# Performance work log

Hardware: AMD Instinct MI355X
Metric: run time of the kernel (lower is better)

Reference implementation:

```python
import math
import jax, jax.numpy as jnp
import numpy as np

B, S, D, H = 2, 2048, 1024, 16
HD = D // H  # 64
EPS = 1e-5


def _layernorm(x, g, b):
    mu = jnp.mean(x, axis=-1, keepdims=True)
    var = jnp.mean(jnp.square(x - mu), axis=-1, keepdims=True)
    return (x - mu) * jax.lax.rsqrt(var + EPS) * g + b


def setup_inputs() -> dict:
    key = jax.random.key(0)
    ks = jax.random.split(key, 16)
    s_attn = 1.0 / math.sqrt(D)
    s_mlp = 1.0 / math.sqrt(4 * D)
    return {
        "hidden_states": jax.random.normal(ks[0], (B, S, D), jnp.float32),
        # MHA params (torch Linear convention: y = x @ W.T + b)
        "Wqkv": jax.random.normal(ks[1], (3 * D, D), jnp.float32) * s_attn,
        "bqkv": jax.random.normal(ks[2], (3 * D,), jnp.float32) * s_attn,
        "Wout": jax.random.normal(ks[3], (D, D), jnp.float32) * s_attn,
        "bout": jax.random.normal(ks[4], (D,), jnp.float32) * s_attn,
        # LayerNorms
        "g1": jnp.ones((D,), jnp.float32),
        "b1": jnp.zeros((D,), jnp.float32),
        "g2": jnp.ones((D,), jnp.float32),
        "b2": jnp.zeros((D,), jnp.float32),
        # MLP (hidden = 4*D, activation = tanh)
        "W1": jax.random.normal(ks[5], (4 * D, D), jnp.float32) * s_attn,
        "bfc1": jax.random.normal(ks[6], (4 * D,), jnp.float32) * s_attn,
        "W2": jax.random.normal(ks[7], (D, 4 * D), jnp.float32) * s_mlp,
        "bfc2": jax.random.normal(ks[8], (D,), jnp.float32) * s_mlp,
    }


def _mha(x, Wqkv, bqkv, Wout, bout):
    # qkv: (B,S,3,H,hd)
    qkv = (x @ Wqkv.T + bqkv).reshape(B, S, 3, H, HD)
    q, k, v = qkv[:, :, 0], qkv[:, :, 1], qkv[:, :, 2]
    # NOTE: source einsum 'bshd,btjd->bsht' contracts over k's head axis j,
    # so each query head attends against sum-over-heads of K (and of V).
    k_sum = k.sum(axis=2)  # (B,S,hd)
    v_sum = v.sum(axis=2)  # (B,S,hd)
    scale = 1.0 / math.sqrt(HD)
    scores = jnp.einsum('bshd,btd->bsht', q, k_sum) * scale  # (B,S,H,S)
    causal = jnp.triu(jnp.ones((S, S), bool), k=1)  # True above diagonal
    scores = jnp.where(causal[None, :, None, :], -jnp.inf, scores)
    attn = jax.nn.softmax(scores, axis=-1)
    out = jnp.einsum('bsht,btd->bshd', attn, v_sum).reshape(B, S, D)
    return out @ Wout.T + bout


def reference(hidden_states, Wqkv, bqkv, Wout, bout, g1, b1, g2, b2, W1, bfc1, W2, bfc2):
    # eval mode: dropouts and stochastic-depth are identity
    residual = hidden_states
    h = _layernorm(residual, g1, b1)
    h = _mha(h, Wqkv, bqkv, Wout, bout)
    residual = h + residual
    h = _layernorm(residual, g2, b2)
    h = jnp.tanh(h @ W1.T + bfc1) @ W2.T + bfc2
    return (h, residual)
```

## Files before the change

kernel.cpp:

```cpp
#include <hip/hip_runtime.h>
#include <hip/hip_bf16.h>

typedef __attribute__((ext_vector_type(8))) short s16x8;
typedef __attribute__((ext_vector_type(4))) float f32x4;
typedef __hip_bfloat16 bf16_t;

__device__ __forceinline__ void gload_lds16(const void* g, void* l) {
  __builtin_amdgcn_global_load_lds(
      (__attribute__((address_space(1))) void*)(g),
      (__attribute__((address_space(3))) void*)(l), 16, 0, 0);
}

__device__ __forceinline__ unsigned cvt_pk_bf16(float lo, float hi) {
  unsigned r;
  asm("v_cvt_pk_bf16_f32 %0, %1, %2" : "=v"(r) : "v"(lo), "v"(hi));
  return r;
}

__device__ __forceinline__ float fast_tanh(float x) {
  float t = exp2f(x * 2.885390082f);
  return 1.0f - 2.0f * __builtin_amdgcn_rcpf(t + 1.0f);
}

__global__ void cast_all_k(const float* __restrict__ Wqkv, const float* __restrict__ Wout,
                           const float* __restrict__ W1, const float* __restrict__ W2,
                           bf16_t* __restrict__ Wqkv_bf, bf16_t* __restrict__ Wout_bf,
                           bf16_t* __restrict__ W1_bf, bf16_t* __restrict__ W2_bf) {
  int c = blockIdx.x * 256 + threadIdx.x;
  const float* src; bf16_t* dst; int off;
  if (c < 131072)      { src = Wqkv; dst = Wqkv_bf; off = c; }
  else if (c < 262144) { src = Wout; dst = Wout_bf; off = c - 131072; }
  else if (c < 786432) { src = W1;   dst = W1_bf;   off = c - 262144; }
  else                 { src = W2;   dst = W2_bf;   off = c - 786432; }
  int i = off * 8;
  float4 a = *(const float4*)(src + i);
  float4 b = *(const float4*)(src + i + 4);
  union { bf16_t h[8]; s16x8 v; } u;
  u.h[0] = __float2bfloat16(a.x); u.h[1] = __float2bfloat16(a.y);
  u.h[2] = __float2bfloat16(a.z); u.h[3] = __float2bfloat16(a.w);
  u.h[4] = __float2bfloat16(b.x); u.h[5] = __float2bfloat16(b.y);
  u.h[6] = __float2bfloat16(b.z); u.h[7] = __float2bfloat16(b.w);
  *(s16x8*)(dst + i) = u.v;
}

__global__ void reduce_kv_k(const float* __restrict__ Wqkv, bf16_t* __restrict__ Wred) {
  int d   = blockIdx.x & 63;
  int isv = blockIdx.x >> 6;
  int col = threadIdx.x * 4;
  const float* base = Wqkv + (size_t)(1024 + isv * 1024 + d) * 1024 + col;
  float4 s = {0.f, 0.f, 0.f, 0.f};
#pragma unroll
  for (int h = 0; h < 16; ++h) {
    float4 t = *(const float4*)(base + (size_t)h * 64 * 1024);
    s.x += t.x; s.y += t.y; s.z += t.z; s.w += t.w;
  }
  union { bf16_t h[4]; uint2 u; } o;
  o.h[0] = __float2bfloat16(s.x); o.h[1] = __float2bfloat16(s.y);
  o.h[2] = __float2bfloat16(s.z); o.h[3] = __float2bfloat16(s.w);
  *(uint2*)(Wred + (size_t)(isv * 64 + d) * 1024 + col) = o.u;
}

__global__ void bias_prep_k(const float* __restrict__ bqkv, float* __restrict__ br) {
  int i = blockIdx.x * 256 + threadIdx.x;
  if (i >= 1152) return;
  if (i < 1024) { br[i] = bqkv[i]; return; }
  int d = i - 1024;
  int off = (d < 64) ? (1024 + d) : (2048 + (d - 64));
  float s = 0.f;
#pragma unroll
  for (int h = 0; h < 16; ++h) s += bqkv[off + h * 64];
  br[i] = s;
}

__global__ __launch_bounds__(256) void ln_cast_k(const float* __restrict__ x,
                                                 const float* __restrict__ g,
                                                 const float* __restrict__ bb,
                                                 bf16_t* __restrict__ y) {
  int row = blockIdx.x, tid = threadIdx.x;
  float4 v = *(const float4*)(x + (size_t)row * 1024 + tid * 4);
  float s = v.x + v.y + v.z + v.w;
  float q = v.x * v.x + v.y * v.y + v.z * v.z + v.w * v.w;
#pragma unroll
  for (int off = 1; off < 64; off <<= 1) {
    s += __shfl_xor(s, off, 64);
    q += __shfl_xor(q, off, 64);
  }
  __shared__ float ss[4], qq[4];
  int wave = tid >> 6, lane = tid & 63;
  if (lane == 0) { ss[wave] = s; qq[wave] = q; }
  __syncthreads();
  s = ss[0] + ss[1] + ss[2] + ss[3];
  q = qq[0] + qq[1] + qq[2] + qq[3];
  float mu  = s * (1.0f / 1024.0f);
  float var = q * (1.0f / 1024.0f) - mu * mu;
  float rstd = rsqrtf(var + 1e-5f);
  float4 gg = *(const float4*)(g + tid * 4);
  float4 bv = *(const float4*)(bb + tid * 4);
  union { bf16_t h[4]; uint2 u; } o;
  o.h[0] = __float2bfloat16((v.x - mu) * rstd * gg.x + bv.x);
  o.h[1] = __float2bfloat16((v.y - mu) * rstd * gg.y + bv.y);
  o.h[2] = __float2bfloat16((v.z - mu) * rstd * gg.z + bv.z);
  o.h[3] = __float2bfloat16((v.w - mu) * rstd * gg.w + bv.w);
  *(uint2*)(y + (size_t)row * 1024 + tid * 4) = o.u;
}

template <int EPI>
__global__ __launch_bounds__(512) void gemm256(
    const bf16_t* __restrict__ A, const bf16_t* __restrict__ Bw,
    const float* __restrict__ bias, void* __restrict__ out0,
    int M, int N, int K, int Kslice) {
  __shared__ __align__(16) bf16_t As[2 * 16384];
  __shared__ __align__(16) bf16_t Bs[2 * 16384];
  const int tid  = threadIdx.x;
  const int lane = tid & 63;
  const int wave = tid >> 6;
  const int l15 = lane & 15, lg = lane >> 4;
  const int wm = wave >> 2, wn = wave & 3;

  const unsigned nx = gridDim.x, ny = gridDim.y;
  unsigned fid = (blockIdx.z * ny + blockIdx.y) * nx + blockIdx.x;
  const unsigned nwg = nx * ny * gridDim.z;
  fid = (fid & 7) * (nwg >> 3) + (fid >> 3);
  const unsigned bxu = fid % nx;
  const unsigned rem = fid / nx;
  const unsigned byu = rem % ny;
  const unsigned bzu = rem / ny;
  const int bm = byu * 256, bn = bxu * 256;
  const size_t Kz = (size_t)K;
  const int kstart = bzu * Kslice;

  f32x4 acc[8][4];
#pragma unroll
  for (int f = 0; f < 8; ++f)
#pragma unroll
    for (int g = 0; g < 4; ++g) acc[f][g] = (f32x4){0.f, 0.f, 0.f, 0.f};

  const bf16_t* Ab = A + (size_t)bm * Kz + kstart;
  const bf16_t* Bb = Bw + (size_t)bn * Kz + kstart;

  const int srow = (tid & 7);
  auto stage = [&](int t, int buf) {
    const int k0 = t * 64;
#pragma unroll
    for (int j = 0; j < 4; ++j) {
      const int c   = j * 512 + tid;
      const int row = c >> 3;
      const int kc  = (c & 7) ^ (row & 7);
      gload_lds16(Ab + (size_t)row * Kz + k0 + kc * 8,
                  As + buf * 16384 + (j * 512 + wave * 64) * 8);
      gload_lds16(Bb + (size_t)row * Kz + k0 + kc * 8,
                  Bs + buf * 16384 + (j * 512 + wave * 64) * 8);
    }
  };
  (void)srow;

  const int NT = Kslice >> 6;
  stage(0, 0);
  int buf = 0;
  for (int t = 0; t < NT; ++t) {
    asm volatile("s_waitcnt vmcnt(0)" ::: "memory");
    __builtin_amdgcn_s_barrier();
    if (t + 1 < NT) stage(t + 1, buf ^ 1);
#pragma unroll
    for (int h = 0; h < 2; ++h) {
      s16x8 af[8], bfv[4];
#pragma unroll
      for (int f = 0; f < 8; ++f) {
        const int row = wm * 128 + f * 16 + l15;
        af[f] = *(const s16x8*)&As[buf * 16384 + (row * 8 + ((h * 4 + lg) ^ (l15 & 7))) * 8];
      }
#pragma unroll
      for (int g = 0; g < 4; ++g) {
        const int row = wn * 64 + g * 16 + l15;
        bfv[g] = *(const s16x8*)&Bs[buf * 16384 + (row * 8 + ((h * 4 + lg) ^ (l15 & 7))) * 8];
      }
      __builtin_amdgcn_s_setprio(1);
#pragma unroll
      for (int f = 0; f < 8; ++f)
#pragma unroll
        for (int g = 0; g < 4; ++g)
          acc[f][g] = __builtin_amdgcn_mfma_f32_16x16x32_bf16(af[f], bfv[g], acc[f][g], 0, 0, 0);
      __builtin_amdgcn_s_setprio(0);
    }
    buf ^= 1;
  }

#pragma unroll
  for (int f = 0; f < 8; ++f) {
    const int row0 = bm + wm * 128 + f * 16 + lg * 4;
#pragma unroll
    for (int g = 0; g < 4; ++g) {
      const int col = bn + wn * 64 + g * 16 + l15;
      const float bcol = (EPI == 4) ? 0.f : bias[col];
#pragma unroll
      for (int r = 0; r < 4; ++r) {
        const int rw = row0 + r;
        float c = acc[f][g][r] + bcol;
        if constexpr (EPI == 2) {
          ((bf16_t*)out0)[(size_t)rw * N + col] = __float2bfloat16(fast_tanh(c));
        } else {
          ((bf16_t*)out0)[((size_t)bzu * M + rw) * N + col] = __float2bfloat16(c);
        }
      }
    }
  }
}

template <int EPI>
__global__ __launch_bounds__(256) void gemm64(
    const bf16_t* __restrict__ A, const bf16_t* __restrict__ Bw,
    const float* __restrict__ bias, void* __restrict__ out0,
    const float* __restrict__ resid, bf16_t* __restrict__ oks,
    bf16_t* __restrict__ ovt, int M, int N, int K) {
  __shared__ __align__(16) bf16_t As[2 * 64 * 32];
  __shared__ __align__(16) bf16_t Bs[2 * 128 * 32];
  const int tid  = threadIdx.x;
  const int lane = tid & 63;
  const int wave = tid >> 6;
  const int l15 = lane & 15, lg = lane >> 4;
  const int wr = (wave >> 1) * 32, wc = (wave & 1) * 64;
  const int bm = blockIdx.y * 64, bn = blockIdx.x * 128;
  const size_t Kz = (size_t)K;
  const int srow = lane >> 2;
  const int scol = ((lane & 3) ^ ((lane >> 3) & 3)) * 8;

  f32x4 acc[2][4];
#pragma unroll
  for (int m = 0; m < 2; ++m)
#pragma unroll
    for (int n = 0; n < 4; ++n) acc[m][n] = (f32x4){0.f, 0.f, 0.f, 0.f};

  const bf16_t* Ab = A + (size_t)bm * Kz;
  const bf16_t* Bb = Bw + (size_t)bn * Kz;

  auto stage = [&](int t, int buf) {
    const int k0 = t * 32;
    gload_lds16(Ab + (size_t)(wave * 16 + srow) * Kz + k0 + scol, As + buf * 2048 + wave * 512);
#pragma unroll
    for (int j = 0; j < 2; ++j) {
      const int cw = wave * 2 + j;
      gload_lds16(Bb + (size_t)(cw * 16 + srow) * Kz + k0 + scol, Bs + buf * 4096 + cw * 512);
    }
  };

  const int NT = K >> 5;
  const int rdoff = (lg ^ ((l15 >> 1) & 3)) * 8;
  stage(0, 0);
  __syncthreads();
  int buf = 0;
  for (int t = 0; t < NT; ++t) {
    if (t + 1 < NT) stage(t + 1, buf ^ 1);
    s16x8 af[2], bfv[4];
#pragma unroll
    for (int m = 0; m < 2; ++m)
      af[m] = *(const s16x8*)&As[buf * 2048 + (wr + m * 16 + l15) * 32 + rdoff];
#pragma unroll
    for (int n = 0; n < 4; ++n)
      bfv[n] = *(const s16x8*)&Bs[buf * 4096 + (wc + n * 16 + l15) * 32 + rdoff];
#pragma unroll
    for (int m = 0; m < 2; ++m)
#pragma unroll
      for (int n = 0; n < 4; ++n)
        acc[m][n] = __builtin_amdgcn_mfma_f32_16x16x32_bf16(af[m], bfv[n], acc[m][n], 0, 0, 0);
    __syncthreads();
    buf ^= 1;
  }

#pragma unroll
  for (int m = 0; m < 2; ++m) {
    const int row0 = bm + wr + m * 16 + lg * 4;
#pragma unroll
    for (int n = 0; n < 4; ++n) {
      const int col = bn + wc + n * 16 + l15;
      const float bcol = bias[col];
#pragma unroll
      for (int r = 0; r < 4; ++r) {
        const int rw = row0 + r;
        float c = acc[m][n][r] + bcol;
        if constexpr (EPI == 0) {
          if (col < 1024) {
            ((bf16_t*)out0)[(size_t)rw * 1024 + col] =
                __float2bfloat16(c * 0.1803368801f);
          } else if (col < 1088) {
            int d = col - 1024, b = rw >> 11, t = rw & 2047;
            oks[((size_t)(b << 11) + t) * 64 + d] = __float2bfloat16(c);
          } else {
            int d = col - 1088, b = rw >> 11, t = rw & 2047;
            ovt[((size_t)b * 64 + d) * 2048 + t] = __float2bfloat16(c);
          }
        } else {
          ((float*)out0)[(size_t)rw * N + col] = c + resid[(size_t)rw * N + col];
        }
      }
    }
  }
}

__global__ __launch_bounds__(256) void fc2_reduce_k(const bf16_t* __restrict__ p,
                                                    const float* __restrict__ bias,
                                                    float* __restrict__ out) {
  const size_t PL = (size_t)4096 * 1024;
  size_t i = ((size_t)blockIdx.x * 256 + threadIdx.x) * 8;
  float acc[8];
  {
    union { s16x8 v; bf16_t h[8]; } u;
    u.v = *(const s16x8*)(p + i);
#pragma unroll
    for (int j = 0; j < 8; ++j) acc[j] = __bfloat162float(u.h[j]);
  }
#pragma unroll
  for (int z = 1; z < 4; ++z) {
    union { s16x8 v; bf16_t h[8]; } u;
    u.v = *(const s16x8*)(p + z * PL + i);
#pragma unroll
    for (int j = 0; j < 8; ++j) acc[j] += __bfloat162float(u.h[j]);
  }
  const int col = (int)(i & 1023);
#pragma unroll
  for (int j = 0; j < 8; ++j) acc[j] += bias[col + j];
  *(float4*)(out + i)     = (float4){acc[0], acc[1], acc[2], acc[3]};
  *(float4*)(out + i + 4) = (float4){acc[4], acc[5], acc[6], acc[7]};
}


template <bool MASK>
__device__ __forceinline__ void attn_tile(
    int t0, int p, const s16x8 (&qf)[2],
    const bf16_t* __restrict__ Ks, const bf16_t* __restrict__ Vs,
    bf16_t* __restrict__ Pl, int l15, int lg,
    float& m_run, float& l_part, f32x4 (&ao)[4]) {
  const int sw7 = l15 & 7;

  f32x4 sc[4];
#pragma unroll
  for (int n = 0; n < 4; ++n) sc[n] = (f32x4){0.f, 0.f, 0.f, 0.f};
#pragma unroll
  for (int ks2 = 0; ks2 < 2; ++ks2) {
#pragma unroll
    for (int n = 0; n < 4; ++n) {
      s16x8 kf = *(const s16x8*)&Ks[(n * 16 + l15) * 64 + (((ks2 << 2) | lg) ^ sw7) * 8];
      sc[n] = __builtin_amdgcn_mfma_f32_16x16x32_bf16(kf, qf[ks2], sc[n], 0, 0, 0);
    }
  }

  float mx = -1e30f;
#pragma unroll
  for (int n = 0; n < 4; ++n) {
#pragma unroll
    for (int r = 0; r < 4; ++r) {
      float v = sc[n][r];
      if (MASK && (t0 + n * 16 + lg * 4 + r > p)) v = -1e30f;
      sc[n][r] = v;
      mx = fmaxf(mx, v);
    }
  }
  if (__any(mx > m_run + 11.5f)) {
    float mxf = fmaxf(mx, __shfl_xor(mx, 16, 64));
    mxf = fmaxf(mxf, __shfl_xor(mxf, 32, 64));
    float mn = fmaxf(m_run, mxf);
    float alpha = exp2f(m_run - mn);
    m_run = mn;
    l_part *= alpha;
#pragma unroll
    for (int r = 0; r < 4; ++r) {
      float ar = __shfl(alpha, lg * 4 + r, 64);
#pragma unroll
      for (int n2 = 0; n2 < 4; ++n2) ao[n2][r] *= ar;
    }
  }
#pragma unroll
  for (int n = 0; n < 4; ++n) {
    float e0 = exp2f(sc[n][0] - m_run);
    float e1 = exp2f(sc[n][1] - m_run);
    float e2 = exp2f(sc[n][2] - m_run);
    float e3 = exp2f(sc[n][3] - m_run);
    l_part += (e0 + e1) + (e2 + e3);
    uint2 d;
    d.x = cvt_pk_bf16(e0, e1);
    d.y = cvt_pk_bf16(e2, e3);
    *(uint2*)&Pl[l15 * 72 + n * 16 + lg * 4] = d;
  }
#pragma unroll
  for (int ks2 = 0; ks2 < 2; ++ks2) {
    s16x8 pa = *(const s16x8*)&Pl[l15 * 72 + ks2 * 32 + lg * 8];
#pragma unroll
    for (int n2 = 0; n2 < 4; ++n2) {
      s16x8 vf = *(const s16x8*)&Vs[(n2 * 16 + l15) * 64 + (((ks2 << 2) | lg) ^ sw7) * 8];
      ao[n2] = __builtin_amdgcn_mfma_f32_16x16x32_bf16(pa, vf, ao[n2], 0, 0, 0);
    }
  }
}

__global__ __launch_bounds__(512) void attn_k(const bf16_t* __restrict__ q,
                                              const bf16_t* __restrict__ ksp,
                                              const bf16_t* __restrict__ vtp,
                                              bf16_t* __restrict__ o) {
  __shared__ __align__(16) bf16_t Ks[3 * 4096];
  __shared__ __align__(16) bf16_t Vs[3 * 4096];
  __shared__ __align__(16) bf16_t Plds[8][16 * 72];
  const int tid = threadIdx.x, lane = tid & 63, wave = tid >> 6;
  const int l15 = lane & 15, lg = lane >> 4;
  const int grp = blockIdx.x >> 1;
  const int b   = blockIdx.x & 1;
  const int pbase = 2040 - 8 * grp;
  const int p = pbase + wave;

  const bf16_t* qb_b = q   + (size_t)b * 32768 * 64;
  const bf16_t* ksb  = ksp + (size_t)b * 2048 * 64;
  const bf16_t* vtb  = vtp + (size_t)b * 64 * 2048;
  bf16_t*       ob   = o   + (size_t)b * 32768 * 64;
  bf16_t* Pl = &Plds[wave][0];

  const int srow = lane >> 3;
  const int scol = lane & 7;
  const int grow = wave * 8 + srow;
  const int gcol = scol ^ (grow & 7);
  const bf16_t* ksrc0 = ksb + (size_t)grow * 64 + gcol * 8;
  const bf16_t* vsrc0 = vtb + (size_t)grow * 2048 + gcol * 8;

  auto stageKV = [&](int t, int buf) {
    const int t0 = t * 64;
    gload_lds16(ksrc0 + (size_t)t0 * 64, Ks + buf * 4096 + wave * 512);
    gload_lds16(vsrc0 + t0, Vs + buf * 4096 + wave * 512);
  };

  s16x8 qf[2];
  {
    const bf16_t* qptr = qb_b + (size_t)(16 * p + l15) * 64;
    qf[0] = *(const s16x8*)(qptr + lg * 8);
    qf[1] = *(const s16x8*)(qptr + 32 + lg * 8);
  }

  float m_run = -1e30f, l_part = 0.f;
  f32x4 ao[4];
#pragma unroll
  for (int n = 0; n < 4; ++n) ao[n] = (f32x4){0.f, 0.f, 0.f, 0.f};

  const int nst = (pbase + 71) >> 6;
  stageKV(0, 0);
  if (nst > 1) stageKV(1, 1);
  int b0 = 0, b1 = 1, b2 = 2;
  for (int tt = 0; tt < nst; ++tt) {
    if (tt + 1 < nst) asm volatile("s_waitcnt vmcnt(2)" ::: "memory");
    else              asm volatile("s_waitcnt vmcnt(0)" ::: "memory");
    __builtin_amdgcn_s_barrier();
    if (tt + 2 < nst) stageKV(tt + 2, b2);
    const int t0 = tt * 64;
    if (t0 <= p) {
      const bf16_t* Kc = Ks + b0 * 4096;
      const bf16_t* Vc = Vs + b0 * 4096;
      if (t0 + 63 <= p)
        attn_tile<false>(t0, p, qf, Kc, Vc, Pl, l15, lg, m_run, l_part, ao);
      else
        attn_tile<true>(t0, p, qf, Kc, Vc, Pl, l15, lg, m_run, l_part, ao);
    }
    int tmp = b0; b0 = b1; b1 = b2; b2 = tmp;
  }

  float l2 = l_part + __shfl_xor(l_part, 16, 64);
  l2 += __shfl_xor(l2, 32, 64);
  float rl[4];
#pragma unroll
  for (int r = 0; r < 4; ++r) rl[r] = 1.0f / __shfl(l2, lg * 4 + r, 64);
#pragma unroll
  for (int n2 = 0; n2 < 4; ++n2) {
#pragma unroll
    for (int r = 0; r < 4; ++r) {
      const int row = 16 * p + lg * 4 + r;
      ob[(size_t)row * 64 + n2 * 16 + l15] = __float2bfloat16(ao[n2][r] * rl[r]);
    }
  }
}

extern "C" void kernel_launch(void* const* d_in, const int* in_sizes, int n_in,
                              void* d_out, int out_size, void* d_ws, size_t ws_size,
                              hipStream_t stream) {
  (void)in_sizes; (void)n_in; (void)out_size; (void)ws_size;
  const float* hidden = (const float*)d_in[0];
  const float* Wqkv   = (const float*)d_in[1];
  const float* bqkv   = (const float*)d_in[2];
  const float* Wout   = (const float*)d_in[3];
  const float* bout   = (const float*)d_in[4];
  const float* g1     = (const float*)d_in[5];
  const float* b1     = (const float*)d_in[6];
  const float* g2     = (const float*)d_in[7];
  const float* b2     = (const float*)d_in[8];
  const float* W1     = (const float*)d_in[9];
  const float* bfc1   = (const float*)d_in[10];
  const float* W2     = (const float*)d_in[11];
  const float* bfc2   = (const float*)d_in[12];

  float* out_h   = (float*)d_out;
  float* out_res = out_h + (size_t)4096 * 1024;

  char* ws = (char*)d_ws;
  auto alloc = [&](size_t bytes) {
    char* p = ws;
    ws += (bytes + 255) & ~(size_t)255;
    return p;
  };
  bf16_t* X1      = (bf16_t*)alloc((size_t)4096 * 1024 * 2);
  bf16_t* Wqkv_bf = (bf16_t*)alloc((size_t)1152 * 1024 * 2);
  float*  bias_r  = (float*)alloc(1152 * 4);
  bf16_t* qb      = (bf16_t*)alloc((size_t)4096 * 1024 * 2);
  bf16_t* ksum    = (bf16_t*)alloc((size_t)2 * 2048 * 64 * 2);
  bf16_t* vT      = (bf16_t*)alloc((size_t)2 * 64 * 2048 * 2);
  bf16_t* Ob      = (bf16_t*)alloc((size_t)4096 * 1024 * 2);
  bf16_t* Wout_bf = (bf16_t*)alloc((size_t)1024 * 1024 * 2);
  bf16_t* X2      = (bf16_t*)alloc((size_t)4096 * 1024 * 2);
  bf16_t* W1_bf   = (bf16_t*)alloc((size_t)4096 * 1024 * 2);
  bf16_t* W2_bf   = (bf16_t*)alloc((size_t)1024 * 4096 * 2);
  bf16_t* H1      = (bf16_t*)alloc((size_t)4096 * 4096 * 2);
  bf16_t* fc2_part = (bf16_t*)d_ws;

  cast_all_k<<<5120, 256, 0, stream>>>(Wqkv, Wout, W1, W2, Wqkv_bf, Wout_bf, W1_bf, W2_bf);
  reduce_kv_k<<<128, 256, 0, stream>>>(Wqkv, Wqkv_bf + (size_t)1024 * 1024);
  bias_prep_k<<<5, 256, 0, stream>>>(bqkv, bias_r);

  ln_cast_k<<<4096, 256, 0, stream>>>(hidden, g1, b1, X1);
  gemm64<0><<<dim3(9, 64), 256, 0, stream>>>(X1, Wqkv_bf, bias_r, qb, nullptr, ksum, vT,
                                             4096, 1152, 1024);
  attn_k<<<512, 512, 0, stream>>>(qb, ksum, vT, Ob);
  gemm64<1><<<dim3(8, 64), 256, 0, stream>>>(Ob, Wout_bf, bout, out_res, hidden, nullptr,
                                             nullptr, 4096, 1024, 1024);
  ln_cast_k<<<4096, 256, 0, stream>>>(out_res, g2, b2, X2);
  gemm256<2><<<dim3(16, 16), 512, 0, stream>>>(X2, W1_bf, bfc1, H1, 4096, 4096, 1024, 1024);
  gemm256<4><<<dim3(4, 16, 4), 512, 0, stream>>>(H1, W2_bf, nullptr, fc2_part,
                                                 4096, 1024, 4096, 1024);
  fc2_reduce_k<<<2048, 256, 0, stream>>>(fc2_part, bfc2, out_h);
}
```

Measured before the change: 212.6 us.

## Pair low and high causal query rows per attention block to share K/V tiles

The attention kernel now gives each block one low query group and its mirrored high group, so the causal work per block is balanced and every staged K/V tile feeds two sets of MFMAs. The grid drops from 512 to 256 blocks. The K/V staging goes from triple to double buffering, and the launch-bounds occupancy hint is raised. In exchange, register pressure roughly doubles for the accumulators, and pipelining depth is reduced.

```diff
diff --git a/kernel.cpp b/kernel.cpp
--- a/kernel.cpp
+++ b/kernel.cpp
@@ -138,7 +138,6 @@
   const bf16_t* Ab = A + (size_t)bm * Kz + kstart;
   const bf16_t* Bb = Bw + (size_t)bn * Kz + kstart;
 
-  const int srow = (tid & 7);
   auto stage = [&](int t, int buf) {
     const int k0 = t * 64;
 #pragma unroll
@@ -152,7 +151,6 @@
                   Bs + buf * 16384 + (j * 512 + wave * 64) * 8);
     }
   };
-  (void)srow;
 
   const int NT = Kslice >> 6;
   stage(0, 0);
@@ -324,25 +322,9 @@
 
 
 template <bool MASK>
-__device__ __forceinline__ void attn_tile(
-    int t0, int p, const s16x8 (&qf)[2],
-    const bf16_t* __restrict__ Ks, const bf16_t* __restrict__ Vs,
-    bf16_t* __restrict__ Pl, int l15, int lg,
+__device__ __forceinline__ void softmax_store(
+    f32x4 (&sc)[4], int t0, int p, bf16_t* __restrict__ Pl, int l15, int lg,
     float& m_run, float& l_part, f32x4 (&ao)[4]) {
-  const int sw7 = l15 & 7;
-
-  f32x4 sc[4];
-#pragma unroll
-  for (int n = 0; n < 4; ++n) sc[n] = (f32x4){0.f, 0.f, 0.f, 0.f};
-#pragma unroll
-  for (int ks2 = 0; ks2 < 2; ++ks2) {
-#pragma unroll
-    for (int n = 0; n < 4; ++n) {
-      s16x8 kf = *(const s16x8*)&Ks[(n * 16 + l15) * 64 + (((ks2 << 2) | lg) ^ sw7) * 8];
-      sc[n] = __builtin_amdgcn_mfma_f32_16x16x32_bf16(kf, qf[ks2], sc[n], 0, 0, 0);
-    }
-  }
-
   float mx = -1e30f;
 #pragma unroll
   for (int n = 0; n < 4; ++n) {
@@ -380,36 +362,71 @@
     d.y = cvt_pk_bf16(e2, e3);
     *(uint2*)&Pl[l15 * 72 + n * 16 + lg * 4] = d;
   }
+}
+
+template <bool LO, bool MLO, bool MHI>
+__device__ __forceinline__ void attn_tile2(
+    int t0, int p_lo, int p_hi,
+    const s16x8 (&qlo)[2], const s16x8 (&qhi)[2],
+    const bf16_t* __restrict__ Ks, const bf16_t* __restrict__ Vs,
+    bf16_t* __restrict__ Pl_lo, bf16_t* __restrict__ Pl_hi, int l15, int lg,
+    float& m_lo, float& l_lo, f32x4 (&ao_lo)[4],
+    float& m_hi, float& l_hi, f32x4 (&ao_hi)[4]) {
+  const int sw7 = l15 & 7;
+
+  f32x4 sl[4], sh[4];
+#pragma unroll
+  for (int n = 0; n < 4; ++n) {
+    sl[n] = (f32x4){0.f, 0.f, 0.f, 0.f};
+    sh[n] = (f32x4){0.f, 0.f, 0.f, 0.f};
+  }
 #pragma unroll
   for (int ks2 = 0; ks2 < 2; ++ks2) {
-    s16x8 pa = *(const s16x8*)&Pl[l15 * 72 + ks2 * 32 + lg * 8];
+#pragma unroll
+    for (int n = 0; n < 4; ++n) {
+      s16x8 kf = *(const s16x8*)&Ks[(n * 16 + l15) * 64 + (((ks2 << 2) | lg) ^ sw7) * 8];
+      sh[n] = __builtin_amdgcn_mfma_f32_16x16x32_bf16(kf, qhi[ks2], sh[n], 0, 0, 0);
+      if (LO) sl[n] = __builtin_amdgcn_mfma_f32_16x16x32_bf16(kf, qlo[ks2], sl[n], 0, 0, 0);
+    }
+  }
+
+  softmax_store<MHI>(sh, t0, p_hi, Pl_hi, l15, lg, m_hi, l_hi, ao_hi);
+  if (LO) softmax_store<MLO>(sl, t0, p_lo, Pl_lo, l15, lg, m_lo, l_lo, ao_lo);
+
+#pragma unroll
+  for (int ks2 = 0; ks2 < 2; ++ks2) {
+    s16x8 pa_h = *(const s16x8*)&Pl_hi[l15 * 72 + ks2 * 32 + lg * 8];
+    s16x8 pa_l;
+    if (LO) pa_l = *(const s16x8*)&Pl_lo[l15 * 72 + ks2 * 32 + lg * 8];
 #pragma unroll
     for (int n2 = 0; n2 < 4; ++n2) {
       s16x8 vf = *(const s16x8*)&Vs[(n2 * 16 + l15) * 64 + (((ks2 << 2) | lg) ^ sw7) * 8];
-      ao[n2] = __builtin_amdgcn_mfma_f32_16x16x32_bf16(pa, vf, ao[n2], 0, 0, 0);
-    }
-  }
-}
-
-__global__ __launch_bounds__(512) void attn_k(const bf16_t* __restrict__ q,
-                                              const bf16_t* __restrict__ ksp,
-                                              const bf16_t* __restrict__ vtp,
-                                              bf16_t* __restrict__ o) {
-  __shared__ __align__(16) bf16_t Ks[3 * 4096];
-  __shared__ __align__(16) bf16_t Vs[3 * 4096];
-  __shared__ __align__(16) bf16_t Plds[8][16 * 72];
+      ao_hi[n2] = __builtin_amdgcn_mfma_f32_16x16x32_bf16(pa_h, vf, ao_hi[n2], 0, 0, 0);
+      if (LO) ao_lo[n2] = __builtin_amdgcn_mfma_f32_16x16x32_bf16(pa_l, vf, ao_lo[n2], 0, 0, 0);
+    }
+  }
+}
+
+__global__ __launch_bounds__(512, 4) void attn_k(const bf16_t* __restrict__ q,
+                                                 const bf16_t* __restrict__ ksp,
+                                                 const bf16_t* __restrict__ vtp,
+                                                 bf16_t* __restrict__ o) {
+  __shared__ __align__(16) bf16_t Ks[2 * 4096];
+  __shared__ __align__(16) bf16_t Vs[2 * 4096];
+  __shared__ __align__(16) bf16_t Plds[8][2][16 * 72];
   const int tid = threadIdx.x, lane = tid & 63, wave = tid >> 6;
   const int l15 = lane & 15, lg = lane >> 4;
-  const int grp = blockIdx.x >> 1;
-  const int b   = blockIdx.x & 1;
-  const int pbase = 2040 - 8 * grp;
-  const int p = pbase + wave;
+  const int g = blockIdx.x >> 1;
+  const int b = blockIdx.x & 1;
+  const int p_lo = 8 * g + wave;
+  const int p_hi = 2040 - 8 * g + wave;
 
   const bf16_t* qb_b = q   + (size_t)b * 32768 * 64;
   const bf16_t* ksb  = ksp + (size_t)b * 2048 * 64;
   const bf16_t* vtb  = vtp + (size_t)b * 64 * 2048;
   bf16_t*       ob   = o   + (size_t)b * 32768 * 64;
-  bf16_t* Pl = &Plds[wave][0];
+  bf16_t* Pl_lo = &Plds[wave][0][0];
+  bf16_t* Pl_hi = &Plds[wave][1][0];
 
   const int srow = lane >> 3;
   const int scol = lane & 7;
@@ -424,52 +441,71 @@
     gload_lds16(vsrc0 + t0, Vs + buf * 4096 + wave * 512);
   };
 
-  s16x8 qf[2];
+  s16x8 qlo[2], qhi[2];
   {
-    const bf16_t* qptr = qb_b + (size_t)(16 * p + l15) * 64;
-    qf[0] = *(const s16x8*)(qptr + lg * 8);
-    qf[1] = *(const s16x8*)(qptr + 32 + lg * 8);
-  }
-
-  float m_run = -1e30f, l_part = 0.f;
-  f32x4 ao[4];
-#pragma unroll
-  for (int n = 0; n < 4; ++n) ao[n] = (f32x4){0.f, 0.f, 0.f, 0.f};
-
-  const int nst = (pbase + 71) >> 6;
+    const bf16_t* ql = qb_b + (size_t)(16 * p_lo + l15) * 64;
+    const bf16_t* qh = qb_b + (size_t)(16 * p_hi + l15) * 64;
+    qlo[0] = *(const s16x8*)(ql + lg * 8);
+    qlo[1] = *(const s16x8*)(ql + 32 + lg * 8);
+    qhi[0] = *(const s16x8*)(qh + lg * 8);
+    qhi[1] = *(const s16x8*)(qh + 32 + lg * 8);
+  }
+
+  float m_lo = -1e30f, l_lo = 0.f, m_hi = -1e30f, l_hi = 0.f;
+  f32x4 ao_lo[4], ao_hi[4];
+#pragma unroll
+  for (int n = 0; n < 4; ++n) {
+    ao_lo[n] = (f32x4){0.f, 0.f, 0.f, 0.f};
+    ao_hi[n] = (f32x4){0.f, 0.f, 0.f, 0.f};
+  }
+
+  const int nst = (2111 - 8 * g) >> 6;
   stageKV(0, 0);
-  if (nst > 1) stageKV(1, 1);
-  int b0 = 0, b1 = 1, b2 = 2;
+  int buf = 0;
   for (int tt = 0; tt < nst; ++tt) {
-    if (tt + 1 < nst) asm volatile("s_waitcnt vmcnt(2)" ::: "memory");
-    else              asm volatile("s_waitcnt vmcnt(0)" ::: "memory");
+    asm volatile("s_waitcnt vmcnt(0)" ::: "memory");
     __builtin_amdgcn_s_barrier();
-    if (tt + 2 < nst) stageKV(tt + 2, b2);
+    if (tt + 1 < nst) stageKV(tt + 1, buf ^ 1);
     const int t0 = tt * 64;
-    if (t0 <= p) {
-      const bf16_t* Kc = Ks + b0 * 4096;
-      const bf16_t* Vc = Vs + b0 * 4096;
-      if (t0 + 63 <= p)
-        attn_tile<false>(t0, p, qf, Kc, Vc, Pl, l15, lg, m_run, l_part, ao);
-      else
-        attn_tile<true>(t0, p, qf, Kc, Vc, Pl, l15, lg, m_run, l_part, ao);
-    }
-    int tmp = b0; b0 = b1; b1 = b2; b2 = tmp;
-  }
-
-  float l2 = l_part + __shfl_xor(l_part, 16, 64);
-  l2 += __shfl_xor(l2, 32, 64);
-  float rl[4];
-#pragma unroll
-  for (int r = 0; r < 4; ++r) rl[r] = 1.0f / __shfl(l2, lg * 4 + r, 64);
-#pragma unroll
-  for (int n2 = 0; n2 < 4; ++n2) {
-#pragma unroll
-    for (int r = 0; r < 4; ++r) {
-      const int row = 16 * p + lg * 4 + r;
-      ob[(size_t)row * 64 + n2 * 16 + l15] = __float2bfloat16(ao[n2][r] * rl[r]);
-    }
-  }
+    const bf16_t* Kc = Ks + buf * 4096;
+    const bf16_t* Vc = Vs + buf * 4096;
+    const bool hiM = (t0 + 63 > p_hi);
+    if (t0 + 63 <= p_lo) {
+      if (hiM) attn_tile2<true, false, true>(t0, p_lo, p_hi, qlo, qhi, Kc, Vc, Pl_lo, Pl_hi,
+                                             l15, lg, m_lo, l_lo, ao_lo, m_hi, l_hi, ao_hi);
+      else     attn_tile2<true, false, false>(t0, p_lo, p_hi, qlo, qhi, Kc, Vc, Pl_lo, Pl_hi,
+                                              l15, lg, m_lo, l_lo, ao_lo, m_hi, l_hi, ao_hi);
+    } else if (t0 <= p_lo) {
+      if (hiM) attn_tile2<true, true, true>(t0, p_lo, p_hi, qlo, qhi, Kc, Vc, Pl_lo, Pl_hi,
+                                            l15, lg, m_lo, l_lo, ao_lo, m_hi, l_hi, ao_hi);
+      else     attn_tile2<true, true, false>(t0, p_lo, p_hi, qlo, qhi, Kc, Vc, Pl_lo, Pl_hi,
+                                             l15, lg, m_lo, l_lo, ao_lo, m_hi, l_hi, ao_hi);
+    } else {
+      if (hiM) attn_tile2<false, false, true>(t0, p_lo, p_hi, qlo, qhi, Kc, Vc, Pl_lo, Pl_hi,
+                                              l15, lg, m_lo, l_lo, ao_lo, m_hi, l_hi, ao_hi);
+      else     attn_tile2<false, false, false>(t0, p_lo, p_hi, qlo, qhi, Kc, Vc, Pl_lo, Pl_hi,
+                                               l15, lg, m_lo, l_lo, ao_lo, m_hi, l_hi, ao_hi);
+    }
+    buf ^= 1;
+  }
+
+  auto finalize = [&](float l_part, f32x4 (&ao)[4], int p) {
+    float l2 = l_part + __shfl_xor(l_part, 16, 64);
+    l2 += __shfl_xor(l2, 32, 64);
+    float rl[4];
+#pragma unroll
+    for (int r = 0; r < 4; ++r) rl[r] = 1.0f / __shfl(l2, lg * 4 + r, 64);
+#pragma unroll
+    for (int n2 = 0; n2 < 4; ++n2) {
+#pragma unroll
+      for (int r = 0; r < 4; ++r) {
+        const int row = 16 * p + lg * 4 + r;
+        ob[(size_t)row * 64 + n2 * 16 + l15] = __float2bfloat16(ao[n2][r] * rl[r]);
+      }
+    }
+  };
+  finalize(l_lo, ao_lo, p_lo);
+  finalize(l_hi, ao_hi, p_hi);
 }
 
 extern "C" void kernel_launch(void* const* d_in, const int* in_sizes, int n_in,
@@ -520,7 +556,7 @@
   ln_cast_k<<<4096, 256, 0, stream>>>(hidden, g1, b1, X1);
   gemm64<0><<<dim3(9, 64), 256, 0, stream>>>(X1, Wqkv_bf, bias_r, qb, nullptr, ksum, vT,
                                              4096, 1152, 1024);
-  attn_k<<<512, 512, 0, stream>>>(qb, ksum, vT, Ob);
+  attn_k<<<256, 512, 0, stream>>>(qb, ksum, vT, Ob);
   gemm64<1><<<dim3(8, 64), 256, 0, stream>>>(Ob, Wout_bf, bout, out_res, hidden, nullptr,
                                              nullptr, 4096, 1024, 1024);
   ln_cast_k<<<4096, 256, 0, stream>>>(out_res, g2, b2, X2);
```

After: 217.5 us. 2.3% more time.
